# Performance work log

Measured on AMD Instinct MI355X. Metric: run time of the kernel, lower is better.

## Reference

```python
import jax, jax.numpy as jnp
import numpy as np

B, N, C = 4, 1024, 1024
H = 16
D = C // H  # 64
HID = int(int(C * 4.0) * 2 / 3)  # 2730
EPS = 1e-6


def rmsnorm(x, w):
    return x * jax.lax.rsqrt(jnp.mean(x * x, axis=-1, keepdims=True) + EPS) * w


def rope_cos_sin(n, d):
    inv_freq = 1.0 / (10000.0 ** (jnp.arange(0, d, 2, dtype=jnp.float32) / d))
    t = jnp.arange(n, dtype=jnp.float32)
    freqs = jnp.einsum('i,j->ij', t, inv_freq)  # [N, D/2]
    emb = jnp.concatenate([freqs, freqs], axis=-1)  # [N, D]
    return jnp.cos(emb), jnp.sin(emb)


def rotate_half(x):
    x1, x2 = jnp.split(x, 2, axis=-1)
    return jnp.concatenate([-x2, x1], axis=-1)


def setup_inputs() -> dict:
    key = jax.random.key(0)
    ks = jax.random.split(key, 12)
    s = lambda fan_in: 1.0 / np.sqrt(fan_in)
    return {
        'x': jax.random.normal(ks[0], (B, N, C), jnp.float32),
        'c': jax.random.normal(ks[1], (B, C), jnp.float32),
        'norm1_w': jnp.ones((C,), jnp.float32),
        'norm2_w': jnp.ones((C,), jnp.float32),
        'qkv_w': jax.random.normal(ks[2], (C, 3 * C), jnp.float32) * s(C),
        'proj_w': jax.random.normal(ks[3], (C, C), jnp.float32) * s(C),
        'proj_b': jnp.zeros((C,), jnp.float32),
        'qn_w': jnp.ones((D,), jnp.float32),
        'kn_w': jnp.ones((D,), jnp.float32),
        'w1': jax.random.normal(ks[4], (C, HID), jnp.float32) * s(C),
        'w2': jax.random.normal(ks[5], (HID, C), jnp.float32) * s(HID),
        'w3': jax.random.normal(ks[6], (C, HID), jnp.float32) * s(C),
        'ada_w': jax.random.normal(ks[7], (C, 6 * C), jnp.float32) * s(C),
        'ada_b': jnp.zeros((6 * C,), jnp.float32),
    }


def reference(x, c, norm1_w, norm2_w, qkv_w, proj_w, proj_b, qn_w, kn_w, w1, w2, w3, ada_w, ada_b):
    # AdaLN modulation params from conditioning
    mods = jax.nn.silu(c) @ ada_w + ada_b  # [B, 6C]
    sh_msa, sc_msa, g_msa, sh_mlp, sc_mlp, g_mlp = jnp.split(mods, 6, axis=-1)

    # --- attention branch ---
    x_mod = rmsnorm(x, norm1_w) * (1 + sc_msa[:, None, :]) + sh_msa[:, None, :]
    qkv = (x_mod @ qkv_w).reshape(B, N, 3, H, D).transpose(2, 0, 3, 1, 4)  # [3,B,H,N,D]
    q, k, v = qkv[0], qkv[1], qkv[2]
    q = rmsnorm(q, qn_w)
    k = rmsnorm(k, kn_w)
    cos, sin = rope_cos_sin(N, D)  # [N, D]
    q = q * cos + rotate_half(q) * sin
    k = k * cos + rotate_half(k) * sin
    attn = jax.nn.softmax(jnp.einsum('bhqd,bhkd->bhqk', q, k) * (D ** -0.5), axis=-1)
    o = jnp.einsum('bhqk,bhkd->bhqd', attn, v).transpose(0, 2, 1, 3).reshape(B, N, C)
    x = x + g_msa[:, None, :] * (o @ proj_w + proj_b)

    # --- SwiGLU MLP branch ---
    x_mod = rmsnorm(x, norm2_w) * (1 + sc_mlp[:, None, :]) + sh_mlp[:, None, :]
    mlp = (jax.nn.silu(x_mod @ w1) * (x_mod @ w3)) @ w2
    x = x + g_mlp[:, None, :] * mlp
    return x
```

## Files before the change

kernel.cpp:

```cpp
#include <hip/hip_runtime.h>
#include <hip/hip_bf16.h>
#include <stdint.h>

using bf16 = __hip_bfloat16;
using bf16x8 = __attribute__((ext_vector_type(8))) short;
using f32x4  = __attribute__((ext_vector_type(4))) float;
using short4v = __attribute__((ext_vector_type(4))) short;

#define EPSF 1e-6f

__device__ __forceinline__ unsigned short f2bu(float x) {
  union { bf16 h; unsigned short u; } cvt;
  cvt.h = __float2bfloat16(x);
  return cvt.u;
}

typedef __attribute__((address_space(3))) void as3_void;
typedef const __attribute__((address_space(1))) void as1_void;

__device__ __forceinline__ void gload_lds16(const void* g, void* l) {
  as1_void* gp = (as1_void*)(uintptr_t)g;
  as3_void* lp = (as3_void*)(uint32_t)(uintptr_t)l;
  __builtin_amdgcn_global_load_lds(gp, lp, 16, 0, 0);
}

__global__ void rope_tab(float* __restrict__ cosT, float* __restrict__ sinT) {
  const int i = blockIdx.x * 256 + threadIdx.x;
  const int n = i >> 5, fi = i & 31;
  const float invf = powf(10000.f, -(float)fi * (1.f / 32.f));
  const float ang = (float)n * invf;
  cosT[i] = cosf(ang);
  sinT[i] = sinf(ang);
}

__global__ void __launch_bounds__(256) ada_part(const float* __restrict__ cc,
                                                const float* __restrict__ adaw,
                                                float* __restrict__ part) {
  __shared__ float sc[256];
  __shared__ float red[1024];
  const int t = threadIdx.x;
  const int cb = blockIdx.x % 48, ks = blockIdx.x / 48;
  const int k0 = ks * 64;
  {
    const int b = t >> 6, kk = t & 63;
    const float v = cc[b * 1024 + k0 + kk];
    sc[t] = v / (1.f + __expf(-v));
  }
  __syncthreads();
  const int colL = t & 127, kh = t >> 7;
  const int col = cb * 128 + colL;
  float a0 = 0.f, a1 = 0.f, a2 = 0.f, a3 = 0.f;
  const float* ap = adaw + (size_t)(k0 + kh * 32) * 6144 + col;
#pragma unroll
  for (int k = 0; k < 32; ++k) {
    const float awv = ap[(size_t)k * 6144];
    const int kk = kh * 32 + k;
    a0 += sc[kk] * awv; a1 += sc[64 + kk] * awv;
    a2 += sc[128 + kk] * awv; a3 += sc[192 + kk] * awv;
  }
  red[kh * 512 + 0 * 128 + colL] = a0;
  red[kh * 512 + 1 * 128 + colL] = a1;
  red[kh * 512 + 2 * 128 + colL] = a2;
  red[kh * 512 + 3 * 128 + colL] = a3;
  __syncthreads();
  if (kh == 0) {
#pragma unroll
    for (int b = 0; b < 4; ++b) {
      const float s = red[b * 128 + colL] + red[512 + b * 128 + colL];
      part[(size_t)(ks * 4 + b) * 6144 + col] = s;
    }
  }
}

__global__ void __launch_bounds__(256) ada_reduce(const float* __restrict__ part,
                                                  const float* __restrict__ adab,
                                                  float* __restrict__ mods) {
  const int i = blockIdx.x * 256 + threadIdx.x;
  const int b = i / 6144, col = i % 6144;
  float s = adab[col];
#pragma unroll
  for (int ks = 0; ks < 16; ++ks) s += part[(size_t)(ks * 4 + b) * 6144 + col];
  mods[b * 6144 + col] = s;
}

__global__ void __launch_bounds__(256) norm_mod(const float* __restrict__ X,
                                                const float* __restrict__ wgt,
                                                const float* __restrict__ mods,
                                                int sh_off, int sc_off,
                                                bf16* __restrict__ Y) {
  __shared__ float red[4];
  const int row = blockIdx.x, t = threadIdx.x, l = t & 63, wv = t >> 6;
  const float4 xv = ((const float4*)(X + (size_t)row * 1024))[t];
  float ss = xv.x * xv.x + xv.y * xv.y + xv.z * xv.z + xv.w * xv.w;
#pragma unroll
  for (int off = 1; off < 64; off <<= 1) ss += __shfl_xor(ss, off);
  if (l == 0) red[wv] = ss;
  __syncthreads();
  ss = (red[0] + red[1]) + (red[2] + red[3]);
  const float rs = rsqrtf(ss * (1.f / 1024.f) + EPSF);
  const int b = row >> 10;
  const float* mb = mods + b * 6144;
  const int c0 = t * 4;
  float vals[4] = {xv.x, xv.y, xv.z, xv.w};
  short4v yv;
#pragma unroll
  for (int j = 0; j < 4; j++) {
    const int cc = c0 + j;
    const float y = vals[j] * rs * wgt[cc] * (1.f + mb[sc_off + cc]) + mb[sh_off + cc];
    yv[j] = (short)f2bu(y);
  }
  *(short4v*)(Y + (size_t)row * 1024 + c0) = yv;
}

__global__ void __launch_bounds__(256) transpose_cast(const float* __restrict__ src, int R, int Cc,
                                                      bf16* __restrict__ dst, int ldd) {
  __shared__ float tile[32][33];
  const int tx = threadIdx.x & 31, ty = threadIdx.x >> 5;
  const int ct = blockIdx.x * 32, rt = blockIdx.y * 32;
#pragma unroll
  for (int kk = 0; kk < 4; ++kk) {
    const int r = rt + ty + kk * 8;
    float v = 0.f;
    if (r < R && (ct + tx) < Cc) v = src[(size_t)r * Cc + ct + tx];
    tile[ty + kk * 8][tx] = v;
  }
  __syncthreads();
#pragma unroll
  for (int kk = 0; kk < 4; ++kk) {
    const int c = ct + ty + kk * 8;
    const int r = rt + tx;
    if (c < Cc && r < ldd) dst[(size_t)c * ldd + r] = __float2bfloat16(tile[tx][ty + kk * 8]);
  }
}

template <int TN, int EPI>
__global__ void __launch_bounds__(256, 3) gemm_p(const bf16* __restrict__ A, int lda,
                                                 const bf16* __restrict__ Bt, int ldb,
                                                 int K, int Nreal, int ldc, int nx,
                                                 bf16* __restrict__ outb,
                                                 float* __restrict__ outf,
                                                 const float* __restrict__ resid,
                                                 const float* __restrict__ gate,
                                                 const float* __restrict__ bias,
                                                 const bf16* __restrict__ h1, int ldh) {
  constexpr int BUFSZ = 8192 + TN * 64;
  constexpr int WN = (TN == 128) ? 2 : 1;
  constexpr int MI = (TN == 128) ? 4 : 2;
  constexpr int WTM = (TN == 128) ? 64 : 32;
  __shared__ char smB[3 * BUFSZ];
  const int t = threadIdx.x, l = t & 63, w = t >> 6;
  const int g = l >> 4, cl = l & 15;
  const int cpx = gridDim.x >> 3;
  const int wg = blockIdx.x;
  const int swz0 = (wg & 7) * cpx + (wg >> 3);
  const int m0 = (swz0 / nx) * 128, n0 = (swz0 % nx) * TN;
  const int wm = w / WN, wn = w % WN;
  f32x4 acc[MI][4] = {};
  const int NK = K >> 5;
  const int srow = t >> 2;
  const int scol = (((t & 3) ^ ((t >> 3) & 3))) * 8;
  const int rsw = (cl >> 1) & 3;

  auto stage = [&](int kt, int buf) {
    char* dst = smB + buf * BUFSZ;
    const int kk = kt * 32 + scol;
    gload_lds16(A + (size_t)(m0 + srow) * lda + kk,      dst + t * 16);
    gload_lds16(A + (size_t)(m0 + 64 + srow) * lda + kk, dst + 4096 + t * 16);
    gload_lds16(Bt + (size_t)(n0 + srow) * ldb + kk,     dst + 8192 + t * 16);
    if constexpr (TN == 128)
      gload_lds16(Bt + (size_t)(n0 + 64 + srow) * ldb + kk, dst + 12288 + t * 16);
  };

  stage(0, 0);
  stage(1, 1);
  if constexpr (TN == 128) asm volatile("s_waitcnt vmcnt(4)" ::: "memory");
  else                     asm volatile("s_waitcnt vmcnt(3)" ::: "memory");
  __builtin_amdgcn_s_barrier();
  __builtin_amdgcn_sched_barrier(0);
  int cur = 0;
  for (int kt = 0; kt < NK; ++kt) {
    if (kt + 2 < NK) stage(kt + 2, (cur >= 1) ? cur - 1 : 2);
    const bf16* Ab = (const bf16*)(smB + cur * BUFSZ);
    const bf16* Bb = (const bf16*)(smB + cur * BUFSZ + 8192);
    bf16x8 af[MI], bfr[4];
#pragma unroll
    for (int i = 0; i < MI; i++)
      af[i] = *(const bf16x8*)&Ab[(wm * WTM + i * 16 + cl) * 32 + ((g ^ rsw) << 3)];
#pragma unroll
    for (int i = 0; i < 4; i++)
      bfr[i] = *(const bf16x8*)&Bb[(wn * 64 + i * 16 + cl) * 32 + ((g ^ rsw) << 3)];
    __builtin_amdgcn_s_setprio(1);
#pragma unroll
    for (int mi = 0; mi < MI; mi++)
#pragma unroll
      for (int ni = 0; ni < 4; ni++)
        acc[mi][ni] = __builtin_amdgcn_mfma_f32_16x16x32_bf16(af[mi], bfr[ni], acc[mi][ni], 0, 0, 0);
    __builtin_amdgcn_s_setprio(0);
    if (kt + 2 < NK) {
      if constexpr (TN == 128) asm volatile("s_waitcnt vmcnt(4)" ::: "memory");
      else                     asm volatile("s_waitcnt vmcnt(3)" ::: "memory");
    } else {
      asm volatile("s_waitcnt vmcnt(0)" ::: "memory");
    }
    __builtin_amdgcn_s_barrier();
    __builtin_amdgcn_sched_barrier(0);
    cur = (cur + 1 == 3) ? 0 : cur + 1;
  }
#pragma unroll
  for (int mi = 0; mi < MI; mi++) {
#pragma unroll
    for (int ni = 0; ni < 4; ni++) {
      const int c = n0 + wn * 64 + ni * 16 + cl;
#pragma unroll
      for (int j = 0; j < 4; j++) {
        const int r = m0 + wm * WTM + mi * 16 + g * 4 + j;
        const float v = acc[mi][ni][j];
        if constexpr (EPI == 0) {
          if (c < Nreal) outb[(size_t)r * ldc + c] = __float2bfloat16(v);
        } else if constexpr (EPI == 1) {
          const int b = r >> 10;
          outf[(size_t)r * ldc + c] = resid[(size_t)r * ldc + c] + gate[b * 6144 + c] * (v + bias[c]);
        } else if constexpr (EPI == 3) {
          if (c < Nreal) {
            const float hv = __bfloat162float(h1[(size_t)r * ldh + c]);
            const float sl = hv / (1.f + __expf(-hv));
            outb[(size_t)r * ldc + c] = __float2bfloat16(sl * v);
          } else {
            outb[(size_t)r * ldc + c] = __float2bfloat16(0.f);
          }
        } else if constexpr (EPI == 4) {
          const int b = r >> 10;
          outf[(size_t)r * ldc + c] = resid[(size_t)r * ldc + c] + gate[b * 6144 + c] * v;
        }
      }
    }
  }
}

__global__ void __launch_bounds__(256) qkv_post(const bf16* __restrict__ qkv,
                                                const float* __restrict__ cosT,
                                                const float* __restrict__ sinT,
                                                const float* __restrict__ qnw,
                                                const float* __restrict__ knw,
                                                bf16* __restrict__ Qo, bf16* __restrict__ Ko) {
  const int t = threadIdx.x, l = t & 63, wv = t >> 6;
  const int row = blockIdx.x * 4 + wv;
  const int token = row >> 4, h = row & 15;
  const int b = token >> 10, n = token & 1023;
  const int d = l;
  const bf16* base = qkv + (size_t)token * 3072 + h * 64 + d;
  float q = __bfloat162float(base[0]);
  float k = __bfloat162float(base[1024]);
  float sq = q * q, sk = k * k;
#pragma unroll
  for (int off = 1; off < 64; off <<= 1) {
    sq += __shfl_xor(sq, off);
    sk += __shfl_xor(sk, off);
  }
  q *= rsqrtf(sq * (1.f / 64.f) + EPSF) * qnw[d];
  k *= rsqrtf(sk * (1.f / 64.f) + EPSF) * knw[d];
  const float cs = cosT[n * 32 + (d & 31)];
  const float sn = sinT[n * 32 + (d & 31)];
  const float qx = __shfl_xor(q, 32), kx = __shfl_xor(k, 32);
  const float sgn = (d < 32) ? -1.f : 1.f;
  const float qo = (q * cs + sgn * qx * sn) * 0.125f;
  const float ko = k * cs + sgn * kx * sn;
  const size_t ob = ((size_t)(b * 16 + h) * 1024 + n) * 64 + d;
  Qo[ob] = __float2bfloat16(qo);
  Ko[ob] = __float2bfloat16(ko);
}

__global__ void __launch_bounds__(256) vtrans(const bf16* __restrict__ qkv,
                                              bf16* __restrict__ vbt) {
  __shared__ unsigned short tile[64 * 64];
  const int t = threadIdx.x;
  const int bh = blockIdx.y, nt = blockIdx.x;
  const int b = bh >> 4, h = bh & 15;
  const int n0 = nt * 64;
#pragma unroll
  for (int rep = 0; rep < 2; ++rep) {
    const int ci = t + rep * 256;
    const int r = ci >> 3, dc = ci & 7;
    const bf16x8 v = *(const bf16x8*)(qkv + (size_t)(b * 1024 + n0 + r) * 3072 + 2048 + h * 64 + dc * 8);
#pragma unroll
    for (int j = 0; j < 8; ++j) {
      const int d = dc * 8 + j;
      const int chunk = (r >> 3) ^ (d & 7) ^ ((d >> 3) & 7);
      tile[d * 64 + chunk * 8 + (r & 7)] = (unsigned short)v[j];
    }
  }
  __syncthreads();
#pragma unroll
  for (int rep = 0; rep < 2; ++rep) {
    const int ci = t + rep * 256;
    const int d = ci >> 3, nc = ci & 7;
    const int phys = nc ^ (d & 7) ^ ((d >> 3) & 7);
    const bf16x8 v = *(const bf16x8*)&tile[d * 64 + phys * 8];
    *(bf16x8*)(vbt + (size_t)bh * 65536 + (size_t)d * 1024 + n0 + nc * 8) = v;
  }
}

__global__ void __launch_bounds__(256) attn_fwd(const bf16* __restrict__ Qb,
                                                const bf16* __restrict__ Kb,
                                                const bf16* __restrict__ Vb,
                                                bf16* __restrict__ Ob) {
  __shared__ char KsB[2 * 8192];
  __shared__ char VsB[2 * 8192];
  __shared__ unsigned short Ps[4 * 16 * 64];
  const int t = threadIdx.x, l = t & 63, w = t >> 6;
  const int g = l >> 4, cl = l & 15;
  const int bh = blockIdx.y;
  const int q0 = blockIdx.x * 64;
  const bf16* Qg = Qb + (size_t)bh * 65536;
  const bf16* Kg = Kb + (size_t)bh * 65536;
  const bf16* Vg = Vb + (size_t)bh * 65536;
  const int qrow = q0 + w * 16 + cl;
  const bf16x8 aq0 = *(const bf16x8*)(Qg + (size_t)qrow * 64 + g * 8);
  const bf16x8 aq1 = *(const bf16x8*)(Qg + (size_t)qrow * 64 + 32 + g * 8);
  float mreg = -1e30f, lreg = 0.f;
  f32x4 o[4] = {};
  const int kr_l = w * 8 + (l >> 3);
  const int ku = (l & 7) ^ (l >> 3);
  unsigned short* Pw = Ps + w * 1024;
  const int sxor = cl & 7;

  auto stageKV = [&](int kvt, int buf) {
    const int kv0 = kvt * 64;
    char* kd = KsB + buf * 8192 + w * 1024;
    char* vd = VsB + buf * 8192 + w * 1024;
    gload_lds16(Kg + (size_t)(kv0 + kr_l) * 64 + ku * 8, kd);
    gload_lds16(Kg + (size_t)(kv0 + 32 + kr_l) * 64 + ku * 8, kd + 4096);
    gload_lds16(Vg + (size_t)kr_l * 1024 + kv0 + ku * 8, vd);
    gload_lds16(Vg + (size_t)(kr_l + 32) * 1024 + kv0 + ku * 8, vd + 4096);
  };

  stageKV(0, 0);
  for (int kvt = 0; kvt < 16; ++kvt) {
    const int cb = kvt & 1;
    if (kvt + 1 < 16) {
      stageKV(kvt + 1, cb ^ 1);
      asm volatile("s_waitcnt vmcnt(4)" ::: "memory");
    } else {
      asm volatile("s_waitcnt vmcnt(0)" ::: "memory");
    }
    __builtin_amdgcn_s_barrier();
    __builtin_amdgcn_sched_barrier(0);
    const char* Kt = KsB + cb * 8192;
    const char* Vt = VsB + cb * 8192;
    f32x4 s[4] = {};
#pragma unroll
    for (int ch = 0; ch < 4; ch++) {
      const int rb = (16 * ch + cl) << 7;
      const bf16x8 bk0 = *(const bf16x8*)(Kt + rb + ((g ^ sxor) << 4));
      s[ch] = __builtin_amdgcn_mfma_f32_16x16x32_bf16(bk0, aq0, s[ch], 0, 0, 0);
      const bf16x8 bk1 = *(const bf16x8*)(Kt + rb + (((4 + g) ^ sxor) << 4));
      s[ch] = __builtin_amdgcn_mfma_f32_16x16x32_bf16(bk1, aq1, s[ch], 0, 0, 0);
    }
    float pm = fmaxf(fmaxf(fmaxf(s[0][0], s[0][1]), fmaxf(s[0][2], s[0][3])),
                     fmaxf(fmaxf(s[1][0], s[1][1]), fmaxf(s[1][2], s[1][3])));
    pm = fmaxf(pm, fmaxf(fmaxf(fmaxf(s[2][0], s[2][1]), fmaxf(s[2][2], s[2][3])),
                         fmaxf(fmaxf(s[3][0], s[3][1]), fmaxf(s[3][2], s[3][3]))));
    pm = fmaxf(pm, __shfl_xor(pm, 16));
    pm = fmaxf(pm, __shfl_xor(pm, 32));
    const float nm = fmaxf(mreg, pm);
    const float al = __expf(mreg - nm);
    mreg = nm;
    float rs = 0.f;
#pragma unroll
    for (int ch = 0; ch < 4; ch++) {
      const float p0 = __expf(s[ch][0] - nm);
      const float p1 = __expf(s[ch][1] - nm);
      const float p2 = __expf(s[ch][2] - nm);
      const float p3 = __expf(s[ch][3] - nm);
      rs += (p0 + p1) + (p2 + p3);
      short4v pk;
      pk[0] = (short)f2bu(p0); pk[1] = (short)f2bu(p1);
      pk[2] = (short)f2bu(p2); pk[3] = (short)f2bu(p3);
      const int phys = (2 * ch + (g >> 1)) ^ sxor;
      *(short4v*)&Pw[cl * 64 + phys * 8 + 4 * (g & 1)] = pk;
    }
    rs += __shfl_xor(rs, 16);
    rs += __shfl_xor(rs, 32);
    lreg = lreg * al + rs;
#pragma unroll
    for (int dc = 0; dc < 4; dc++) {
      o[dc][0] *= al; o[dc][1] *= al; o[dc][2] *= al; o[dc][3] *= al;
    }
    const bf16x8 pa0 = *(const bf16x8*)&Pw[cl * 64 + ((g ^ sxor) << 3)];
    const bf16x8 pa1 = *(const bf16x8*)&Pw[cl * 64 + (((4 + g) ^ sxor) << 3)];
#pragma unroll
    for (int dc = 0; dc < 4; dc++) {
      const int vr = (16 * dc + cl) << 7;
      const bf16x8 bv0 = *(const bf16x8*)(Vt + vr + ((g ^ sxor) << 4));
      o[dc] = __builtin_amdgcn_mfma_f32_16x16x32_bf16(bv0, pa0, o[dc], 0, 0, 0);
      const bf16x8 bv1 = *(const bf16x8*)(Vt + vr + (((4 + g) ^ sxor) << 4));
      o[dc] = __builtin_amdgcn_mfma_f32_16x16x32_bf16(bv1, pa1, o[dc], 0, 0, 0);
    }
    __builtin_amdgcn_s_barrier();
  }
  const int b = bh >> 4, h = bh & 15;
  const float inv = 1.f / lreg;
  const int q = q0 + w * 16 + cl;
  const size_t base = ((size_t)(b * 1024 + q) * 16 + h) * 64;
#pragma unroll
  for (int dc = 0; dc < 4; dc++) {
    short4v ov;
    ov[0] = (short)f2bu(o[dc][0] * inv);
    ov[1] = (short)f2bu(o[dc][1] * inv);
    ov[2] = (short)f2bu(o[dc][2] * inv);
    ov[3] = (short)f2bu(o[dc][3] * inv);
    *(short4v*)(Ob + base + 16 * dc + 4 * g) = ov;
  }
}

extern "C" void kernel_launch(void* const* d_in, const int* in_sizes, int n_in,
                              void* d_out, int out_size, void* d_ws, size_t ws_size,
                              hipStream_t stream) {
  const float* x     = (const float*)d_in[0];
  const float* c     = (const float*)d_in[1];
  const float* n1w   = (const float*)d_in[2];
  const float* n2w   = (const float*)d_in[3];
  const float* qkvw  = (const float*)d_in[4];
  const float* projw = (const float*)d_in[5];
  const float* projb = (const float*)d_in[6];
  const float* qnw   = (const float*)d_in[7];
  const float* knw   = (const float*)d_in[8];
  const float* w1    = (const float*)d_in[9];
  const float* w2    = (const float*)d_in[10];
  const float* w3    = (const float*)d_in[11];
  const float* adaw  = (const float*)d_in[12];
  const float* adab  = (const float*)d_in[13];
  float* outp = (float*)d_out;
  char* ws = (char*)d_ws;
  if (ws_size < 93159424u) return;

  float* ropeC = (float*)(ws + 0);
  float* ropeS = (float*)(ws + 131072);
  float* mods  = (float*)(ws + 262144);
  bf16* xmod   = (bf16*)(ws + 360448);
  bf16* qkvwt  = (bf16*)(ws + 8749056);
  bf16* projwt = (bf16*)(ws + 15040512);
  bf16* w1t    = (bf16*)(ws + 17137664);
  bf16* w3t    = (bf16*)(ws + 22904832);
  bf16* w2t    = (bf16*)(ws + 28672000);
  bf16* qkv    = (bf16*)(ws + 34439168);
  float* apart = (float*)(ws + 34439168);
  bf16* h1     = (bf16*)(ws + 34439168);
  bf16* qb     = (bf16*)(ws + 59604992);
  bf16* gbuf   = (bf16*)(ws + 59604992);
  bf16* kb     = (bf16*)(ws + 67993600);
  bf16* vbt    = (bf16*)(ws + 76382208);
  bf16* ob     = (bf16*)(ws + 84770816);

  rope_tab<<<128, 256, 0, stream>>>(ropeC, ropeS);
  ada_part<<<768, 256, 0, stream>>>(c, adaw, apart);
  ada_reduce<<<96, 256, 0, stream>>>(apart, adab, mods);
  transpose_cast<<<dim3(96, 32), 256, 0, stream>>>(qkvw, 1024, 3072, qkvwt, 1024);
  transpose_cast<<<dim3(32, 32), 256, 0, stream>>>(projw, 1024, 1024, projwt, 1024);
  transpose_cast<<<dim3(86, 32), 256, 0, stream>>>(w1, 1024, 2730, w1t, 1024);
  transpose_cast<<<dim3(86, 32), 256, 0, stream>>>(w3, 1024, 2730, w3t, 1024);
  transpose_cast<<<dim3(32, 88), 256, 0, stream>>>(w2, 2730, 1024, w2t, 2816);

  norm_mod<<<4096, 256, 0, stream>>>(x, n1w, mods, 0, 1024, xmod);
  gemm_p<128, 0><<<768, 256, 0, stream>>>(xmod, 1024, qkvwt, 1024, 1024, 3072, 3072, 24,
                                          qkv, nullptr, nullptr, nullptr, nullptr, nullptr, 0);
  vtrans<<<dim3(16, 64), 256, 0, stream>>>(qkv, vbt);
  qkv_post<<<16384, 256, 0, stream>>>(qkv, ropeC, ropeS, qnw, knw, qb, kb);
  attn_fwd<<<dim3(16, 64), 256, 0, stream>>>(qb, kb, vbt, ob);
  gemm_p<64, 1><<<512, 256, 0, stream>>>(ob, 1024, projwt, 1024, 1024, 1024, 1024, 16,
                                         nullptr, outp, x, mods + 2048, projb, nullptr, 0);

  norm_mod<<<4096, 256, 0, stream>>>(outp, n2w, mods, 3072, 4096, xmod);
  gemm_p<128, 0><<<704, 256, 0, stream>>>(xmod, 1024, w1t, 1024, 1024, 2730, 2816, 22,
                                          h1, nullptr, nullptr, nullptr, nullptr, nullptr, 0);
  gemm_p<128, 3><<<704, 256, 0, stream>>>(xmod, 1024, w3t, 1024, 1024, 2730, 2816, 22,
                                          gbuf, nullptr, nullptr, nullptr, nullptr, h1, 2816);
  gemm_p<64, 4><<<512, 256, 0, stream>>>(gbuf, 2816, w2t, 2816, 2816, 1024, 1024, 16,
                                         nullptr, outp, outp, mods + 5120, nullptr, nullptr, 0);
}
```

Before: 288.7 us.

## Add 256x256-tile 8-wave GEMM kernel for QKV and MLP up-projections

Introduces a new GEMM kernel with 512 threads, 256x256 output tiles, 64-wide K steps in double-buffered 128KB LDS, and staged loads interleaved inside the MFMA loop at quarter-tile granularity. It is used for the QKV, w1 and w3 GEMMs, while the proj and w2 GEMMs keep a specialised 128x64 kernel. Larger tiles raise arithmetic intensity and cut global/LDS traffic per FLOP, at the cost of fewer blocks (176-192 workgroups on 256 CUs) and heavy LDS and register use that limits occupancy.

Result: slower. 302.4 us (+4.7%).

```diff
diff --git a/kernel.cpp b/kernel.cpp
--- a/kernel.cpp
+++ b/kernel.cpp
@@ -133,93 +133,113 @@
   }
 }
 
-template <int TN, int EPI>
-__global__ void __launch_bounds__(256, 3) gemm_p(const bf16* __restrict__ A, int lda,
+template <int EPI>
+__global__ void __launch_bounds__(512, 2) gemm8p(const bf16* __restrict__ A, int lda,
                                                  const bf16* __restrict__ Bt, int ldb,
-                                                 int K, int Nreal, int ldc, int nx,
+                                                 int NKT, int Nreal, int ldc, int nx,
                                                  bf16* __restrict__ outb,
-                                                 float* __restrict__ outf,
-                                                 const float* __restrict__ resid,
-                                                 const float* __restrict__ gate,
-                                                 const float* __restrict__ bias,
                                                  const bf16* __restrict__ h1, int ldh) {
-  constexpr int BUFSZ = 8192 + TN * 64;
-  constexpr int WN = (TN == 128) ? 2 : 1;
-  constexpr int MI = (TN == 128) ? 4 : 2;
-  constexpr int WTM = (TN == 128) ? 64 : 32;
-  __shared__ char smB[3 * BUFSZ];
+  __shared__ char smB[131072];
   const int t = threadIdx.x, l = t & 63, w = t >> 6;
   const int g = l >> 4, cl = l & 15;
+  const int wm = w >> 2, wn = w & 3;
   const int cpx = gridDim.x >> 3;
   const int wg = blockIdx.x;
-  const int swz0 = (wg & 7) * cpx + (wg >> 3);
-  const int m0 = (swz0 / nx) * 128, n0 = (swz0 % nx) * TN;
-  const int wm = w / WN, wn = w % WN;
-  f32x4 acc[MI][4] = {};
-  const int NK = K >> 5;
-  const int srow = t >> 2;
-  const int scol = (((t & 3) ^ ((t >> 3) & 3))) * 8;
-  const int rsw = (cl >> 1) & 3;
-
-  auto stage = [&](int kt, int buf) {
-    char* dst = smB + buf * BUFSZ;
-    const int kk = kt * 32 + scol;
-    gload_lds16(A + (size_t)(m0 + srow) * lda + kk,      dst + t * 16);
-    gload_lds16(A + (size_t)(m0 + 64 + srow) * lda + kk, dst + 4096 + t * 16);
-    gload_lds16(Bt + (size_t)(n0 + srow) * ldb + kk,     dst + 8192 + t * 16);
-    if constexpr (TN == 128)
-      gload_lds16(Bt + (size_t)(n0 + 64 + srow) * ldb + kk, dst + 12288 + t * 16);
+  const int swz = (wg & 7) * cpx + (wg >> 3);
+  const int m0 = (swz / nx) * 256, n0 = (swz % nx) * 256;
+  const int sr = t >> 3;
+  const int sc8 = ((t & 7) ^ (sr & 7)) * 8;
+  const int axor = cl & 7;
+  f32x4 acc[8][4] = {};
+
+  auto stageH = [&](int mat, int tt, int h) {
+    const int base = mat * 65536 + (tt & 1) * 32768 + h * 16384;
+    const bf16* src = mat ? Bt : A;
+    const int ld = mat ? ldb : lda;
+    const int row0 = (mat ? n0 : m0) + h * 128 + sr;
+    const bf16* sp = src + (size_t)row0 * ld + tt * 64 + sc8;
+    gload_lds16(sp, smB + base + t * 16);
+    gload_lds16(sp + (size_t)64 * ld, smB + base + 8192 + t * 16);
   };
 
-  stage(0, 0);
-  stage(1, 1);
-  if constexpr (TN == 128) asm volatile("s_waitcnt vmcnt(4)" ::: "memory");
-  else                     asm volatile("s_waitcnt vmcnt(3)" ::: "memory");
+  stageH(1, 0, 0); stageH(1, 0, 1);
+  stageH(0, 0, 0); stageH(0, 0, 1);
+  stageH(1, 1, 0); stageH(1, 1, 1);
+  asm volatile("s_waitcnt vmcnt(4)" ::: "memory");
   __builtin_amdgcn_s_barrier();
   __builtin_amdgcn_sched_barrier(0);
-  int cur = 0;
-  for (int kt = 0; kt < NK; ++kt) {
-    if (kt + 2 < NK) stage(kt + 2, (cur >= 1) ? cur - 1 : 2);
-    const bf16* Ab = (const bf16*)(smB + cur * BUFSZ);
-    const bf16* Bb = (const bf16*)(smB + cur * BUFSZ + 8192);
-    bf16x8 af[MI], bfr[4];
-#pragma unroll
-    for (int i = 0; i < MI; i++)
-      af[i] = *(const bf16x8*)&Ab[(wm * WTM + i * 16 + cl) * 32 + ((g ^ rsw) << 3)];
-#pragma unroll
-    for (int i = 0; i < 4; i++)
-      bfr[i] = *(const bf16x8*)&Bb[(wn * 64 + i * 16 + cl) * 32 + ((g ^ rsw) << 3)];
-    __builtin_amdgcn_s_setprio(1);
-#pragma unroll
-    for (int mi = 0; mi < MI; mi++)
-#pragma unroll
-      for (int ni = 0; ni < 4; ni++)
-        acc[mi][ni] = __builtin_amdgcn_mfma_f32_16x16x32_bf16(af[mi], bfr[ni], acc[mi][ni], 0, 0, 0);
-    __builtin_amdgcn_s_setprio(0);
-    if (kt + 2 < NK) {
-      if constexpr (TN == 128) asm volatile("s_waitcnt vmcnt(4)" ::: "memory");
-      else                     asm volatile("s_waitcnt vmcnt(3)" ::: "memory");
-    } else {
-      asm volatile("s_waitcnt vmcnt(0)" ::: "memory");
-    }
-    __builtin_amdgcn_s_barrier();
-    __builtin_amdgcn_sched_barrier(0);
-    cur = (cur + 1 == 3) ? 0 : cur + 1;
-  }
-#pragma unroll
-  for (int mi = 0; mi < MI; mi++) {
+
+  const int NI = NKT >> 1;
+  for (int it = 0; it < NI; ++it) {
+    const int t0 = 2 * it;
+    const bool full = (it + 1 < NI);
+#pragma unroll
+    for (int hf = 0; hf < 2; ++hf) {
+      const int tt = t0 + hf;
+      const int pA = (tt & 1) * 32768 + wm * 16384;
+      const int pB = 65536 + (tt & 1) * 32768 + (wn >> 1) * 16384 + (wn & 1) * 8192;
+      bf16x8 bfr[4][2];
+#pragma unroll
+      for (int q = 0; q < 4; ++q) {
+        bf16x8 af[2][2];
+#pragma unroll
+        for (int i = 0; i < 2; ++i)
+#pragma unroll
+          for (int kh = 0; kh < 2; ++kh)
+            af[i][kh] = *(const bf16x8*)(smB + pA + ((2 * q + i) * 16 + cl) * 128 +
+                                         (((kh * 4 + g) ^ axor) << 4));
+        if (q == 0) {
+#pragma unroll
+          for (int n = 0; n < 4; ++n)
+#pragma unroll
+            for (int kh = 0; kh < 2; ++kh)
+              bfr[n][kh] = *(const bf16x8*)(smB + pB + (n * 16 + cl) * 128 +
+                                            (((kh * 4 + g) ^ axor) << 4));
+        }
+        if (hf == 0) {
+          if (q == 0)      stageH(0, t0 + 1, 0);
+          else if (q == 1) stageH(0, t0 + 1, 1);
+          else if (q == 2) { if (full) stageH(1, t0 + 2, 0); }
+          else             { if (full) stageH(1, t0 + 2, 1); }
+        } else {
+          if (q == 0)      { if (full) stageH(0, t0 + 2, 0); }
+          else if (q == 1) { if (full) stageH(0, t0 + 2, 1); }
+          else if (q == 2) { if (full) stageH(1, t0 + 3, 0); }
+          else             { if (full) stageH(1, t0 + 3, 1); }
+        }
+        __builtin_amdgcn_s_barrier();
+        asm volatile("s_waitcnt lgkmcnt(0)" ::: "memory");
+        __builtin_amdgcn_sched_barrier(0);
+        __builtin_amdgcn_s_setprio(1);
+#pragma unroll
+        for (int i = 0; i < 2; ++i)
+#pragma unroll
+          for (int n = 0; n < 4; ++n) {
+            acc[2 * q + i][n] =
+                __builtin_amdgcn_mfma_f32_16x16x32_bf16(af[i][0], bfr[n][0], acc[2 * q + i][n], 0, 0, 0);
+            acc[2 * q + i][n] =
+                __builtin_amdgcn_mfma_f32_16x16x32_bf16(af[i][1], bfr[n][1], acc[2 * q + i][n], 0, 0, 0);
+          }
+        __builtin_amdgcn_s_setprio(0);
+        if (q == 3) {
+          if (full) asm volatile("s_waitcnt vmcnt(4)" ::: "memory");
+          else      asm volatile("s_waitcnt vmcnt(0)" ::: "memory");
+        }
+        __builtin_amdgcn_s_barrier();
+      }
+    }
+  }
+#pragma unroll
+  for (int mi = 0; mi < 8; mi++) {
 #pragma unroll
     for (int ni = 0; ni < 4; ni++) {
       const int c = n0 + wn * 64 + ni * 16 + cl;
 #pragma unroll
       for (int j = 0; j < 4; j++) {
-        const int r = m0 + wm * WTM + mi * 16 + g * 4 + j;
+        const int r = m0 + wm * 128 + mi * 16 + g * 4 + j;
         const float v = acc[mi][ni][j];
         if constexpr (EPI == 0) {
           if (c < Nreal) outb[(size_t)r * ldc + c] = __float2bfloat16(v);
-        } else if constexpr (EPI == 1) {
-          const int b = r >> 10;
-          outf[(size_t)r * ldc + c] = resid[(size_t)r * ldc + c] + gate[b * 6144 + c] * (v + bias[c]);
         } else if constexpr (EPI == 3) {
           if (c < Nreal) {
             const float hv = __bfloat162float(h1[(size_t)r * ldh + c]);
@@ -228,6 +248,85 @@
           } else {
             outb[(size_t)r * ldc + c] = __float2bfloat16(0.f);
           }
+        }
+      }
+    }
+  }
+}
+
+template <int EPI>
+__global__ void __launch_bounds__(256, 3) gemm_p(const bf16* __restrict__ A, int lda,
+                                                 const bf16* __restrict__ Bt, int ldb,
+                                                 int K, int ldc, int nx,
+                                                 float* __restrict__ outf,
+                                                 const float* __restrict__ resid,
+                                                 const float* __restrict__ gate,
+                                                 const float* __restrict__ bias) {
+  constexpr int BUFSZ = 8192 + 4096;
+  __shared__ char smB[3 * BUFSZ];
+  const int t = threadIdx.x, l = t & 63, w = t >> 6;
+  const int g = l >> 4, cl = l & 15;
+  const int cpx = gridDim.x >> 3;
+  const int wg = blockIdx.x;
+  const int swz0 = (wg & 7) * cpx + (wg >> 3);
+  const int m0 = (swz0 / nx) * 128, n0 = (swz0 % nx) * 64;
+  const int wm = w, wn = 0;
+  f32x4 acc[2][4] = {};
+  const int NK = K >> 5;
+  const int srow = t >> 2;
+  const int scol = (((t & 3) ^ ((t >> 3) & 3))) * 8;
+  const int rsw = (cl >> 1) & 3;
+
+  auto stage = [&](int kt, int buf) {
+    char* dst = smB + buf * BUFSZ;
+    const int kk = kt * 32 + scol;
+    gload_lds16(A + (size_t)(m0 + srow) * lda + kk,      dst + t * 16);
+    gload_lds16(A + (size_t)(m0 + 64 + srow) * lda + kk, dst + 4096 + t * 16);
+    gload_lds16(Bt + (size_t)(n0 + srow) * ldb + kk,     dst + 8192 + t * 16);
+  };
+
+  stage(0, 0);
+  stage(1, 1);
+  asm volatile("s_waitcnt vmcnt(3)" ::: "memory");
+  __builtin_amdgcn_s_barrier();
+  __builtin_amdgcn_sched_barrier(0);
+  int cur = 0;
+  for (int kt = 0; kt < NK; ++kt) {
+    if (kt + 2 < NK) stage(kt + 2, (cur >= 1) ? cur - 1 : 2);
+    const bf16* Ab = (const bf16*)(smB + cur * BUFSZ);
+    const bf16* Bb = (const bf16*)(smB + cur * BUFSZ + 8192);
+    bf16x8 af[2], bfr[4];
+#pragma unroll
+    for (int i = 0; i < 2; i++)
+      af[i] = *(const bf16x8*)&Ab[(wm * 32 + i * 16 + cl) * 32 + ((g ^ rsw) << 3)];
+#pragma unroll
+    for (int i = 0; i < 4; i++)
+      bfr[i] = *(const bf16x8*)&Bb[(i * 16 + cl) * 32 + ((g ^ rsw) << 3)];
+    __builtin_amdgcn_s_setprio(1);
+#pragma unroll
+    for (int mi = 0; mi < 2; mi++)
+#pragma unroll
+      for (int ni = 0; ni < 4; ni++)
+        acc[mi][ni] = __builtin_amdgcn_mfma_f32_16x16x32_bf16(af[mi], bfr[ni], acc[mi][ni], 0, 0, 0);
+    __builtin_amdgcn_s_setprio(0);
+    if (kt + 2 < NK) asm volatile("s_waitcnt vmcnt(3)" ::: "memory");
+    else             asm volatile("s_waitcnt vmcnt(0)" ::: "memory");
+    __builtin_amdgcn_s_barrier();
+    __builtin_amdgcn_sched_barrier(0);
+    cur = (cur + 1 == 3) ? 0 : cur + 1;
+  }
+#pragma unroll
+  for (int mi = 0; mi < 2; mi++) {
+#pragma unroll
+    for (int ni = 0; ni < 4; ni++) {
+      const int c = n0 + ni * 16 + cl;
+#pragma unroll
+      for (int j = 0; j < 4; j++) {
+        const int r = m0 + wm * 32 + mi * 16 + g * 4 + j;
+        const float v = acc[mi][ni][j];
+        if constexpr (EPI == 1) {
+          const int b = r >> 10;
+          outf[(size_t)r * ldc + c] = resid[(size_t)r * ldc + c] + gate[b * 6144 + c] * (v + bias[c]);
         } else if constexpr (EPI == 4) {
           const int b = r >> 10;
           outf[(size_t)r * ldc + c] = resid[(size_t)r * ldc + c] + gate[b * 6144 + c] * v;
@@ -462,19 +561,19 @@
   transpose_cast<<<dim3(32, 88), 256, 0, stream>>>(w2, 2730, 1024, w2t, 2816);
 
   norm_mod<<<4096, 256, 0, stream>>>(x, n1w, mods, 0, 1024, xmod);
-  gemm_p<128, 0><<<768, 256, 0, stream>>>(xmod, 1024, qkvwt, 1024, 1024, 3072, 3072, 24,
-                                          qkv, nullptr, nullptr, nullptr, nullptr, nullptr, 0);
+  gemm8p<0><<<192, 512, 0, stream>>>(xmod, 1024, qkvwt, 1024, 16, 3072, 3072, 12,
+                                     qkv, nullptr, 0);
   vtrans<<<dim3(16, 64), 256, 0, stream>>>(qkv, vbt);
   qkv_post<<<16384, 256, 0, stream>>>(qkv, ropeC, ropeS, qnw, knw, qb, kb);
   attn_fwd<<<dim3(16, 64), 256, 0, stream>>>(qb, kb, vbt, ob);
-  gemm_p<64, 1><<<512, 256, 0, stream>>>(ob, 1024, projwt, 1024, 1024, 1024, 1024, 16,
-                                         nullptr, outp, x, mods + 2048, projb, nullptr, 0);
+  gemm_p<1><<<512, 256, 0, stream>>>(ob, 1024, projwt, 1024, 1024, 1024, 16,
+                                     outp, x, mods + 2048, projb);
 
   norm_mod<<<4096, 256, 0, stream>>>(outp, n2w, mods, 3072, 4096, xmod);
-  gemm_p<128, 0><<<704, 256, 0, stream>>>(xmod, 1024, w1t, 1024, 1024, 2730, 2816, 22,
-                                          h1, nullptr, nullptr, nullptr, nullptr, nullptr, 0);
-  gemm_p<128, 3><<<704, 256, 0, stream>>>(xmod, 1024, w3t, 1024, 1024, 2730, 2816, 22,
-                                          gbuf, nullptr, nullptr, nullptr, nullptr, h1, 2816);
-  gemm_p<64, 4><<<512, 256, 0, stream>>>(gbuf, 2816, w2t, 2816, 2816, 1024, 1024, 16,
-                                         nullptr, outp, outp, mods + 5120, nullptr, nullptr, 0);
-}
+  gemm8p<0><<<176, 512, 0, stream>>>(xmod, 1024, w1t, 1024, 16, 2730, 2816, 11,
+                                     h1, nullptr, 0);
+  gemm8p<3><<<176, 512, 0, stream>>>(xmod, 1024, w3t, 1024, 16, 2730, 2816, 11,
+                                     gbuf, h1, 2816);
+  gemm_p<4><<<512, 256, 0, stream>>>(gbuf, 2816, w2t, 2816, 2816, 1024, 16,
+                                     outp, outp, mods + 5120, nullptr);
+}
```

## Fuse W1 and W3 GEMMs into a single dual-accumulator SwiGLU kernel

Applied to the files above, without the earlier changes.

Replaces the two separate MLP up-projection GEMMs (W1, then W3 with a SiLU-gate epilogue reading h1 back from memory) with one kernel that stages A once plus both weight tiles and keeps two accumulator sets. The SwiGLU product is formed in registers, which removes the h1 write and read-back and halves the A-tile loads. The cost is double the accumulator registers and more LDS per block, so occupancy drops (launch bounds 2 instead of 3).

Measured after the change: 266.3 us. 7.8% less time.

```diff
diff --git a/kernel.cpp b/kernel.cpp
--- a/kernel.cpp
+++ b/kernel.cpp
@@ -141,8 +141,7 @@
                                                  float* __restrict__ outf,
                                                  const float* __restrict__ resid,
                                                  const float* __restrict__ gate,
-                                                 const float* __restrict__ bias,
-                                                 const bf16* __restrict__ h1, int ldh) {
+                                                 const float* __restrict__ bias) {
   constexpr int BUFSZ = 8192 + TN * 64;
   constexpr int WN = (TN == 128) ? 2 : 1;
   constexpr int MI = (TN == 128) ? 4 : 2;
@@ -220,17 +219,95 @@
         } else if constexpr (EPI == 1) {
           const int b = r >> 10;
           outf[(size_t)r * ldc + c] = resid[(size_t)r * ldc + c] + gate[b * 6144 + c] * (v + bias[c]);
-        } else if constexpr (EPI == 3) {
-          if (c < Nreal) {
-            const float hv = __bfloat162float(h1[(size_t)r * ldh + c]);
-            const float sl = hv / (1.f + __expf(-hv));
-            outb[(size_t)r * ldc + c] = __float2bfloat16(sl * v);
-          } else {
-            outb[(size_t)r * ldc + c] = __float2bfloat16(0.f);
-          }
         } else if constexpr (EPI == 4) {
           const int b = r >> 10;
           outf[(size_t)r * ldc + c] = resid[(size_t)r * ldc + c] + gate[b * 6144 + c] * v;
+        }
+      }
+    }
+  }
+}
+
+__global__ void __launch_bounds__(256, 2) gemm_w13(const bf16* __restrict__ A, int lda,
+                                                   const bf16* __restrict__ B1t,
+                                                   const bf16* __restrict__ B3t, int ldb,
+                                                   int K, int Nreal, int ldc, int nx,
+                                                   bf16* __restrict__ outb) {
+  constexpr int BUFSZ = 24576;
+  __shared__ char smB[3 * BUFSZ];
+  const int t = threadIdx.x, l = t & 63, w = t >> 6;
+  const int g = l >> 4, cl = l & 15;
+  const int cpx = gridDim.x >> 3;
+  const int wg = blockIdx.x;
+  const int swz0 = (wg & 7) * cpx + (wg >> 3);
+  const int m0 = (swz0 / nx) * 128, n0 = (swz0 % nx) * 128;
+  const int wm = w >> 1, wn = w & 1;
+  f32x4 acc1[4][4] = {}, acc3[4][4] = {};
+  const int NK = K >> 5;
+  const int srow = t >> 2;
+  const int scol = (((t & 3) ^ ((t >> 3) & 3))) * 8;
+  const int rsw = (cl >> 1) & 3;
+
+  auto stage = [&](int kt, int buf) {
+    char* dst = smB + buf * BUFSZ;
+    const int kk = kt * 32 + scol;
+    gload_lds16(A   + (size_t)(m0 + srow) * lda + kk,      dst + t * 16);
+    gload_lds16(A   + (size_t)(m0 + 64 + srow) * lda + kk, dst + 4096 + t * 16);
+    gload_lds16(B1t + (size_t)(n0 + srow) * ldb + kk,      dst + 8192 + t * 16);
+    gload_lds16(B1t + (size_t)(n0 + 64 + srow) * ldb + kk, dst + 12288 + t * 16);
+    gload_lds16(B3t + (size_t)(n0 + srow) * ldb + kk,      dst + 16384 + t * 16);
+    gload_lds16(B3t + (size_t)(n0 + 64 + srow) * ldb + kk, dst + 20480 + t * 16);
+  };
+
+  stage(0, 0);
+  stage(1, 1);
+  asm volatile("s_waitcnt vmcnt(6)" ::: "memory");
+  __builtin_amdgcn_s_barrier();
+  __builtin_amdgcn_sched_barrier(0);
+  int cur = 0;
+  for (int kt = 0; kt < NK; ++kt) {
+    if (kt + 2 < NK) stage(kt + 2, (cur >= 1) ? cur - 1 : 2);
+    const bf16* Ab  = (const bf16*)(smB + cur * BUFSZ);
+    const bf16* B1b = (const bf16*)(smB + cur * BUFSZ + 8192);
+    const bf16* B3b = (const bf16*)(smB + cur * BUFSZ + 16384);
+    bf16x8 af[4], b1r[4], b3r[4];
+#pragma unroll
+    for (int i = 0; i < 4; i++)
+      af[i] = *(const bf16x8*)&Ab[(wm * 64 + i * 16 + cl) * 32 + ((g ^ rsw) << 3)];
+#pragma unroll
+    for (int i = 0; i < 4; i++) {
+      b1r[i] = *(const bf16x8*)&B1b[(wn * 64 + i * 16 + cl) * 32 + ((g ^ rsw) << 3)];
+      b3r[i] = *(const bf16x8*)&B3b[(wn * 64 + i * 16 + cl) * 32 + ((g ^ rsw) << 3)];
+    }
+    __builtin_amdgcn_s_setprio(1);
+#pragma unroll
+    for (int mi = 0; mi < 4; mi++)
+#pragma unroll
+      for (int ni = 0; ni < 4; ni++) {
+        acc1[mi][ni] = __builtin_amdgcn_mfma_f32_16x16x32_bf16(af[mi], b1r[ni], acc1[mi][ni], 0, 0, 0);
+        acc3[mi][ni] = __builtin_amdgcn_mfma_f32_16x16x32_bf16(af[mi], b3r[ni], acc3[mi][ni], 0, 0, 0);
+      }
+    __builtin_amdgcn_s_setprio(0);
+    if (kt + 2 < NK) asm volatile("s_waitcnt vmcnt(6)" ::: "memory");
+    else             asm volatile("s_waitcnt vmcnt(0)" ::: "memory");
+    __builtin_amdgcn_s_barrier();
+    __builtin_amdgcn_sched_barrier(0);
+    cur = (cur + 1 == 3) ? 0 : cur + 1;
+  }
+#pragma unroll
+  for (int mi = 0; mi < 4; mi++) {
+#pragma unroll
+    for (int ni = 0; ni < 4; ni++) {
+      const int c = n0 + wn * 64 + ni * 16 + cl;
+#pragma unroll
+      for (int j = 0; j < 4; j++) {
+        const int r = m0 + wm * 64 + mi * 16 + g * 4 + j;
+        if (c < Nreal) {
+          const float hv = acc1[mi][ni][j];
+          const float sl = hv / (1.f + __expf(-hv));
+          outb[(size_t)r * ldc + c] = __float2bfloat16(sl * acc3[mi][ni][j]);
+        } else {
+          outb[(size_t)r * ldc + c] = __float2bfloat16(0.f);
         }
       }
     }
@@ -445,7 +522,6 @@
   bf16* w2t    = (bf16*)(ws + 28672000);
   bf16* qkv    = (bf16*)(ws + 34439168);
   float* apart = (float*)(ws + 34439168);
-  bf16* h1     = (bf16*)(ws + 34439168);
   bf16* qb     = (bf16*)(ws + 59604992);
   bf16* gbuf   = (bf16*)(ws + 59604992);
   bf16* kb     = (bf16*)(ws + 67993600);
@@ -463,18 +539,16 @@
 
   norm_mod<<<4096, 256, 0, stream>>>(x, n1w, mods, 0, 1024, xmod);
   gemm_p<128, 0><<<768, 256, 0, stream>>>(xmod, 1024, qkvwt, 1024, 1024, 3072, 3072, 24,
-                                          qkv, nullptr, nullptr, nullptr, nullptr, nullptr, 0);
+                                          qkv, nullptr, nullptr, nullptr, nullptr);
   vtrans<<<dim3(16, 64), 256, 0, stream>>>(qkv, vbt);
   qkv_post<<<16384, 256, 0, stream>>>(qkv, ropeC, ropeS, qnw, knw, qb, kb);
   attn_fwd<<<dim3(16, 64), 256, 0, stream>>>(qb, kb, vbt, ob);
   gemm_p<64, 1><<<512, 256, 0, stream>>>(ob, 1024, projwt, 1024, 1024, 1024, 1024, 16,
-                                         nullptr, outp, x, mods + 2048, projb, nullptr, 0);
+                                         nullptr, outp, x, mods + 2048, projb);
 
   norm_mod<<<4096, 256, 0, stream>>>(outp, n2w, mods, 3072, 4096, xmod);
-  gemm_p<128, 0><<<704, 256, 0, stream>>>(xmod, 1024, w1t, 1024, 1024, 2730, 2816, 22,
-                                          h1, nullptr, nullptr, nullptr, nullptr, nullptr, 0);
-  gemm_p<128, 3><<<704, 256, 0, stream>>>(xmod, 1024, w3t, 1024, 1024, 2730, 2816, 22,
-                                          gbuf, nullptr, nullptr, nullptr, nullptr, h1, 2816);
+  gemm_w13<<<704, 256, 0, stream>>>(xmod, 1024, w1t, w3t, 1024, 1024, 2730, 2816, 22,
+                                    gbuf);
   gemm_p<64, 4><<<512, 256, 0, stream>>>(gbuf, 2816, w2t, 2816, 2816, 1024, 1024, 16,
-                                         nullptr, outp, outp, mods + 5120, nullptr, nullptr, 0);
-}
+                                         nullptr, outp, outp, mods + 5120, nullptr);
+}
```
